# Kernel tuning notes

Hardware: AMD Instinct MI355X
Metric: run time of the kernel (lower is better)

Reference implementation:

```python
import jax, jax.numpy as jnp
import numpy as np

NUM_GROUPS = 32
EPS = 1e-6


def group_norm(x, gamma, beta):
    # x: [b, c, n]
    b, c, n = x.shape
    xg = x.reshape(b, NUM_GROUPS, (c // NUM_GROUPS) * n)
    mean = xg.mean(axis=-1, keepdims=True)
    var = xg.var(axis=-1, keepdims=True)
    xg = (xg - mean) * jax.lax.rsqrt(var + EPS)
    x = xg.reshape(b, c, n)
    return x * gamma[None, :, None] + beta[None, :, None]


def conv1x1(x, w, bias):
    # x: [b, c, n], w: [out, in], bias: [out]
    return jnp.einsum('oc,bcn->bon', w, x) + bias[None, :, None]


def setup_inputs() -> dict:
    key = jax.random.key(0)
    ks = jax.random.split(key, 12)
    b, c, n = 16, 512, 2048
    scale = 1.0 / np.sqrt(c)
    inp = {
        'x': jax.random.normal(ks[0], (b, c, n), dtype=jnp.float32),
        'gn_gamma': jnp.ones((c,), dtype=jnp.float32),
        'gn_beta': jnp.zeros((c,), dtype=jnp.float32),
        'wq': jax.random.normal(ks[1], (c, c), dtype=jnp.float32) * scale,
        'bq': jnp.zeros((c,), dtype=jnp.float32),
        'wk': jax.random.normal(ks[2], (c, c), dtype=jnp.float32) * scale,
        'bk': jnp.zeros((c,), dtype=jnp.float32),
        'wv': jax.random.normal(ks[3], (c, c), dtype=jnp.float32) * scale,
        'bv': jnp.zeros((c,), dtype=jnp.float32),
        'wo': jax.random.normal(ks[4], (c, c), dtype=jnp.float32) * scale,
        'bo': jnp.zeros((c,), dtype=jnp.float32),
    }
    return inp


def reference(x, gn_gamma, gn_beta, wq, bq, wk, bk, wv, bv, wo, bo):
    # x: [b, c, n]
    c = x.shape[1]
    h = group_norm(x, gn_gamma, gn_beta)
    q = conv1x1(h, wq, bq)  # [b, c, n]
    k = conv1x1(h, wk, bk)  # [b, c, n]
    v = conv1x1(h, wv, bv)  # [b, c, n]
    # scores: q^T k  -> [b, n_q, n_kv]
    scores = jnp.einsum('bcn,bcm->bnm', q, k) * (c ** -0.5)
    attn = jax.nn.softmax(scores, axis=-1)  # softmax over keys (dim=2)
    # h = v @ attn^T  -> [b, c, n_q]
    out = jnp.einsum('bcm,bnm->bcn', v, attn)
    out = conv1x1(out, wo, bo)
    return x + out
```

## Files before the change

### kernel.cpp

```cpp
#include <hip/hip_runtime.h>
#include <hip/hip_bf16.h>
#include <math.h>

#define Bb 16
#define Cc 512
#define Nn 2048

typedef unsigned short u16;
typedef __attribute__((ext_vector_type(8))) short bf16x8;
typedef __attribute__((ext_vector_type(4))) float f32x4;

typedef __attribute__((address_space(3))) unsigned as3_u32;
typedef __attribute__((address_space(1))) const unsigned as1_u32;

__device__ __forceinline__ float b2f(u16 u){ unsigned x = ((unsigned)u) << 16; return __builtin_bit_cast(float, x); }
__device__ __forceinline__ u16 f2b(float f){
  unsigned x = __builtin_bit_cast(unsigned, f);
  x += 0x7fffu + ((x >> 16) & 1u);
  return (u16)(x >> 16);
}

__device__ __forceinline__ void gload16(const u16* g, u16* l){
  __builtin_amdgcn_global_load_lds((as1_u32*)(uintptr_t)(const void*)g,
                                   (as3_u32*)(uintptr_t)(void*)l, 16, 0, 0);
}

#define BAR() do{ __builtin_amdgcn_s_barrier(); asm volatile("" ::: "memory"); }while(0)
#define WAITV4() asm volatile("s_waitcnt vmcnt(4)" ::: "memory")
#define WAITV0() asm volatile("s_waitcnt vmcnt(0)" ::: "memory")

__global__ __launch_bounds__(256) void k_cvt4(const float* __restrict__ s0, const float* __restrict__ s1,
                                              const float* __restrict__ s2, const float* __restrict__ s3,
                                              u16* __restrict__ d0, u16* __restrict__ d1,
                                              u16* __restrict__ d2, u16* __restrict__ d3){
  int z = blockIdx.z;
  const float* s = (z == 0) ? s0 : (z == 1) ? s1 : (z == 2) ? s2 : s3;
  u16* d = (z == 0) ? d0 : (z == 1) ? d1 : (z == 2) ? d2 : d3;
  int i = blockIdx.x * 256 + threadIdx.x;
  float4 v = ((const float4*)s)[i];
  ushort4 o; o.x = f2b(v.x); o.y = f2b(v.y); o.z = f2b(v.z); o.w = f2b(v.w);
  ((ushort4*)d)[i] = o;
}

__global__ __launch_bounds__(256) void k_gn(const float* __restrict__ x,
                                            const float* __restrict__ gamma,
                                            const float* __restrict__ beta,
                                            u16* __restrict__ h){
  int bid = blockIdx.x;
  int b = bid >> 5, g = bid & 31;
  const float4* xv = (const float4*)(x + ((size_t)b * Cc + g * 16) * Nn);
  u16* hp = h + ((size_t)b * Cc + g * 16) * Nn;
  int t = threadIdx.x;
  float s = 0.f, ss = 0.f;
#pragma unroll 4
  for (int it = 0; it < 32; ++it){
    float4 v = xv[it * 256 + t];
    s  += v.x + v.y + v.z + v.w;
    ss += v.x * v.x + v.y * v.y + v.z * v.z + v.w * v.w;
  }
#pragma unroll
  for (int o = 32; o >= 1; o >>= 1){ s += __shfl_xor(s, o); ss += __shfl_xor(ss, o); }
  __shared__ float rs[4], rss[4];
  int w = t >> 6;
  if ((t & 63) == 0){ rs[w] = s; rss[w] = ss; }
  __syncthreads();
  s  = rs[0] + rs[1] + rs[2] + rs[3];
  ss = rss[0] + rss[1] + rss[2] + rss[3];
  float mean = s * (1.f / 32768.f);
  float var  = ss * (1.f / 32768.f) - mean * mean;
  float inv  = rsqrtf(var + 1e-6f);
#pragma unroll 4
  for (int it = 0; it < 32; ++it){
    int idx = it * 256 + t;
    float4 u = xv[idx];
    int ch = g * 16 + (idx >> 9);
    float ga = gamma[ch] * inv, be = beta[ch];
    ushort4 o;
    o.x = f2b((u.x - mean) * ga + be);
    o.y = f2b((u.y - mean) * ga + be);
    o.z = f2b((u.z - mean) * ga + be);
    o.w = f2b((u.w - mean) * ga + be);
    ((ushort4*)hp)[idx] = o;
  }
}

__global__ __launch_bounds__(256) void k_tr(const u16* __restrict__ h, u16* __restrict__ ht){
  __shared__ u16 lds[64 * 65];
  int b = blockIdx.z;
  int n0 = blockIdx.x * 64, c0 = blockIdx.y * 64;
  const u16* src = h + (size_t)b * Cc * Nn;
  u16* dst = ht + (size_t)b * Nn * Cc;
  int t = threadIdx.x;
  int jc = (t & 7) << 3;
  int r  = t >> 3;
#pragma unroll
  for (int it = 0; it < 2; ++it){
    int rr = r + it * 32;
    uint4 vv = *(const uint4*)(src + (size_t)(c0 + rr) * Nn + n0 + jc);
    u16* pv = (u16*)&vv;
#pragma unroll
    for (int e = 0; e < 8; ++e) lds[(jc + e) * 65 + rr] = pv[e];
  }
  __syncthreads();
#pragma unroll
  for (int it = 0; it < 2; ++it){
    int rn = r + it * 32;
    u16 tmp[8];
#pragma unroll
    for (int e = 0; e < 8; ++e) tmp[e] = lds[rn * 65 + jc + e];
    *(uint4*)(dst + (size_t)(n0 + rn) * Cc + c0 + jc) = *(const uint4*)tmp;
  }
}

#define GSLOT 32768

__device__ __forceinline__ void gemm256(const u16* __restrict__ A, int lda,
                                        const u16* __restrict__ B, int ldb, int K,
                                        u16* __restrict__ lds, f32x4 (&acc)[8][4]){
  const int tid = threadIdx.x;
  const int w = tid >> 6, lane = tid & 63;
  const int lr = lane & 15, lk = lane >> 4;
  const int wr = w >> 2, wc = w & 3;

  const int sw0 = ((lk    ) ^ (lr & 7)) << 3;
  const int sw1 = ((lk + 4) ^ (lr & 7)) << 3;
  const int arow = (wr * 128 + lr) * 64;
  const int brow = 16384 + (wc * 64 + lr) * 64;

  const int r0 = tid >> 3, c0 = tid & 7;
  const size_t offA0 = (size_t)r0 * lda + (size_t)((c0 ^ (r0 & 7)) << 3);
  const size_t offA1 = offA0 + (size_t)64 * lda;
  const size_t offB0 = (size_t)r0 * ldb + (size_t)((c0 ^ (r0 & 7)) << 3);
  const size_t offB1 = offB0 + (size_t)64 * ldb;
  const int d0 = tid * 8, d1 = tid * 8 + 4096;

#define STGA(h, T, bu) do{ const u16* gp = A + (size_t)(T) * 64 + (size_t)(h) * 128 * lda; \
    u16* lp = lds + (bu) * GSLOT + (h) * 8192; \
    gload16(gp + offA0, lp + d0); gload16(gp + offA1, lp + d1); }while(0)
#define STGB(h, T, bu) do{ const u16* gp = B + (size_t)(T) * 64 + (size_t)(h) * 128 * ldb; \
    u16* lp = lds + (bu) * GSLOT + 16384 + (h) * 8192; \
    gload16(gp + offB0, lp + d0); gload16(gp + offB1, lp + d1); }while(0)

#pragma unroll
  for (int i = 0; i < 8; ++i)
#pragma unroll
    for (int j = 0; j < 4; ++j){ f32x4 z = {0.f,0.f,0.f,0.f}; acc[i][j] = z; }

  const int NT = K >> 6;

  STGA(0, 0, 0); STGA(1, 0, 0); STGB(0, 0, 0); STGB(1, 0, 0);
  if (NT > 1){ STGB(0, 1, 1); STGA(0, 1, 1); WAITV4(); }
  else { WAITV0(); }
  BAR();

  bf16x8 a[4][2], b[4][2];

#pragma unroll 1
  for (int T = 0; T < NT; ++T){
    const u16* cur = lds + (T & 1) * GSLOT;
    const int nb = (T + 1) & 1, cb = T & 1;
    const bool p1 = (T + 1) < NT, p2 = (T + 2) < NT;

#pragma unroll
    for (int i = 0; i < 4; ++i){
      a[i][0] = *(const bf16x8*)(cur + arow + i * 1024 + sw0);
      a[i][1] = *(const bf16x8*)(cur + arow + i * 1024 + sw1);
    }
#pragma unroll
    for (int j = 0; j < 2; ++j){
      b[j][0] = *(const bf16x8*)(cur + brow + j * 1024 + sw0);
      b[j][1] = *(const bf16x8*)(cur + brow + j * 1024 + sw1);
    }
    if (p1) STGB(1, T + 1, nb);
    BAR();
    __builtin_amdgcn_s_setprio(1);
#pragma unroll
    for (int i = 0; i < 4; ++i)
#pragma unroll
      for (int j = 0; j < 2; ++j)
#pragma unroll
        for (int ks = 0; ks < 2; ++ks)
          acc[i][j] = __builtin_amdgcn_mfma_f32_16x16x32_bf16(b[j][ks], a[i][ks], acc[i][j], 0, 0, 0);
    __builtin_amdgcn_s_setprio(0);
    BAR();

#pragma unroll
    for (int j = 2; j < 4; ++j){
      b[j][0] = *(const bf16x8*)(cur + brow + j * 1024 + sw0);
      b[j][1] = *(const bf16x8*)(cur + brow + j * 1024 + sw1);
    }
    if (p1) STGA(1, T + 1, nb);
    BAR();
    __builtin_amdgcn_s_setprio(1);
#pragma unroll
    for (int i = 0; i < 4; ++i)
#pragma unroll
      for (int j = 2; j < 4; ++j)
#pragma unroll
        for (int ks = 0; ks < 2; ++ks)
          acc[i][j] = __builtin_amdgcn_mfma_f32_16x16x32_bf16(b[j][ks], a[i][ks], acc[i][j], 0, 0, 0);
    __builtin_amdgcn_s_setprio(0);
    BAR();

#pragma unroll
    for (int i = 0; i < 4; ++i){
      a[i][0] = *(const bf16x8*)(cur + arow + 4096 + i * 1024 + sw0);
      a[i][1] = *(const bf16x8*)(cur + arow + 4096 + i * 1024 + sw1);
    }
    if (p2) STGB(0, T + 2, cb);
    BAR();
    __builtin_amdgcn_s_setprio(1);
#pragma unroll
    for (int i = 0; i < 4; ++i)
#pragma unroll
      for (int j = 0; j < 2; ++j)
#pragma unroll
        for (int ks = 0; ks < 2; ++ks)
          acc[4 + i][j] = __builtin_amdgcn_mfma_f32_16x16x32_bf16(b[j][ks], a[i][ks], acc[4 + i][j], 0, 0, 0);
    __builtin_amdgcn_s_setprio(0);
    BAR();

    if (p2) STGA(0, T + 2, cb);
    BAR();
    __builtin_amdgcn_s_setprio(1);
#pragma unroll
    for (int i = 0; i < 4; ++i)
#pragma unroll
      for (int j = 2; j < 4; ++j)
#pragma unroll
        for (int ks = 0; ks < 2; ++ks)
          acc[4 + i][j] = __builtin_amdgcn_mfma_f32_16x16x32_bf16(b[j][ks], a[i][ks], acc[4 + i][j], 0, 0, 0);
    __builtin_amdgcn_s_setprio(0);
    if (p2){ WAITV4(); } else if (p1){ WAITV0(); }
    BAR();
  }
#undef STGA
#undef STGB
}

#define EPI_COORDS \
  int lane = threadIdx.x & 63, w = threadIdx.x >> 6; \
  int wr = w >> 2, wc = w & 3; \
  int lr = lane & 15; \
  int lk = lane >> 4; \
  int g4 = lk << 2; \
  (void)lk;

__global__ __launch_bounds__(512, 2) void k_qkv(const u16* __restrict__ ht,
                                                const u16* __restrict__ wqb, const u16* __restrict__ wkb,
                                                const u16* __restrict__ wvb,
                                                const float* __restrict__ bq, const float* __restrict__ bk,
                                                const float* __restrict__ bv,
                                                u16* __restrict__ qt, u16* __restrict__ kt,
                                                u16* __restrict__ v){
  __shared__ u16 lds[2 * GSLOT];
  int bid = blockIdx.x;
  int id = (bid & 7) * 96 + (bid >> 3);
  f32x4 acc[8][4];
  if (id < 512){
    int b = id >> 5, r = id & 31;
    int p = r >> 4, t = r & 15;
    int m0 = (t & 7) * 256, n0 = (t >> 3) * 256;
    const u16* A = ht + (size_t)b * Nn * Cc + (size_t)m0 * Cc;
    const u16* B = (p ? wkb : wqb) + (size_t)n0 * Cc;
    const float* bias = p ? bk : bq;
    u16* out = (p ? kt : qt) + (size_t)b * Nn * Cc;
    gemm256(A, Cc, B, Cc, Cc, lds, acc);
    EPI_COORDS
#pragma unroll
    for (int i = 0; i < 8; ++i){
      int row = m0 + wr * 128 + i * 16 + lr;
#pragma unroll
      for (int j = 0; j < 4; ++j){
        int coln = n0 + wc * 64 + j * 16 + g4;
        float4 bi = *(const float4*)(bias + coln);
        ushort4 o;
        o.x = f2b(acc[i][j][0] + bi.x);
        o.y = f2b(acc[i][j][1] + bi.y);
        o.z = f2b(acc[i][j][2] + bi.z);
        o.w = f2b(acc[i][j][3] + bi.w);
        *(ushort4*)(out + (size_t)row * Cc + coln) = o;
      }
    }
  } else {
    int u = id - 512;
    int b = u >> 4, r = u & 15;
    int m0 = (r & 1) * 256, n0 = (r >> 1) * 256;
    const u16* A = wvb + (size_t)m0 * Cc;
    const u16* B = ht + (size_t)b * Nn * Cc + (size_t)n0 * Cc;
    u16* out = v + (size_t)b * Cc * Nn;
    gemm256(A, Cc, B, Cc, Cc, lds, acc);
    EPI_COORDS
#pragma unroll
    for (int i = 0; i < 8; ++i){
      int row = m0 + wr * 128 + i * 16 + lr;
      float bi = bv[row];
#pragma unroll
      for (int j = 0; j < 4; ++j){
        int coln = n0 + wc * 64 + j * 16 + g4;
        ushort4 o;
        o.x = f2b(acc[i][j][0] + bi);
        o.y = f2b(acc[i][j][1] + bi);
        o.z = f2b(acc[i][j][2] + bi);
        o.w = f2b(acc[i][j][3] + bi);
        *(ushort4*)(out + (size_t)row * Nn + coln) = o;
      }
    }
  }
}

__global__ __launch_bounds__(512, 2) void k_scores(const u16* __restrict__ qt, const u16* __restrict__ kt,
                                                   u16* __restrict__ p, float* __restrict__ lsum){
  __shared__ u16 lds[2 * GSLOT];
  __shared__ float sums[256][4];
  int bid = blockIdx.x;
  int swz = (bid & 7) * 128 + (bid >> 3);
  int b = swz >> 6, rem = swz & 63;
  int m0 = (rem & 7) * 256, n0 = (rem >> 3) * 256;
  const u16* A = qt + (size_t)b * Nn * Cc + (size_t)m0 * Cc;
  const u16* B = kt + (size_t)b * Nn * Cc + (size_t)n0 * Cc;
  u16* pb = p + (size_t)b * Nn * Nn;
  f32x4 acc[8][4];
  gemm256(A, Cc, B, Cc, Cc, lds, acc);
  const float scale = 0.044194173824159216f;
  EPI_COORDS
  float psum[8];
#pragma unroll
  for (int i = 0; i < 8; ++i) psum[i] = 0.f;
#pragma unroll
  for (int i = 0; i < 8; ++i){
    int row = m0 + wr * 128 + i * 16 + lr;
#pragma unroll
    for (int j = 0; j < 4; ++j){
      int coln = n0 + wc * 64 + j * 16 + g4;
      float e0 = __expf(acc[i][j][0] * scale);
      float e1 = __expf(acc[i][j][1] * scale);
      float e2 = __expf(acc[i][j][2] * scale);
      float e3 = __expf(acc[i][j][3] * scale);
      psum[i] += (e0 + e1) + (e2 + e3);
      ushort4 o; o.x = f2b(e0); o.y = f2b(e1); o.z = f2b(e2); o.w = f2b(e3);
      *(ushort4*)(pb + (size_t)row * Nn + coln) = o;
    }
  }
#pragma unroll
  for (int i = 0; i < 8; ++i){
    psum[i] += __shfl_xor(psum[i], 16);
    psum[i] += __shfl_xor(psum[i], 32);
  }
  if (lk == 0){
#pragma unroll
    for (int i = 0; i < 8; ++i) sums[wr * 128 + i * 16 + lr][wc] = psum[i];
  }
  __syncthreads();
  int tid = threadIdx.x;
  if (tid < 256){
    float sv = sums[tid][0] + sums[tid][1] + sums[tid][2] + sums[tid][3];
    atomicAdd(lsum + (size_t)b * Nn + m0 + tid, sv);
  }
}

__global__ __launch_bounds__(512, 2) void k_pv(const u16* __restrict__ p, const u16* __restrict__ v,
                                               const float* __restrict__ lsum, u16* __restrict__ aot){
  __shared__ u16 lds[2 * GSLOT];
  int bid = blockIdx.x;
  int swz = (bid & 7) * 32 + (bid >> 3);
  int b = swz >> 4, rem = swz & 15;
  int m0 = (rem & 7) * 256, n0 = (rem >> 3) * 256;
  const u16* A = p + (size_t)b * Nn * Nn + (size_t)m0 * Nn;
  const u16* B = v + (size_t)b * Cc * Nn + (size_t)n0 * Nn;
  u16* out = aot + (size_t)b * Nn * Cc;
  f32x4 acc[8][4];
  gemm256(A, Nn, B, Nn, Nn, lds, acc);
  EPI_COORDS
#pragma unroll
  for (int i = 0; i < 8; ++i){
    int row = m0 + wr * 128 + i * 16 + lr;
    float linv = 1.0f / lsum[(size_t)b * Nn + row];
#pragma unroll
    for (int j = 0; j < 4; ++j){
      int coln = n0 + wc * 64 + j * 16 + g4;
      ushort4 o;
      o.x = f2b(acc[i][j][0] * linv);
      o.y = f2b(acc[i][j][1] * linv);
      o.z = f2b(acc[i][j][2] * linv);
      o.w = f2b(acc[i][j][3] * linv);
      *(ushort4*)(out + (size_t)row * Cc + coln) = o;
    }
  }
}

__global__ __launch_bounds__(512, 2) void k_proj(const u16* __restrict__ wob, const u16* __restrict__ aot,
                                                 const float* __restrict__ bo, const float* __restrict__ x,
                                                 float* __restrict__ out){
  __shared__ u16 lds[2 * GSLOT];
  int b = blockIdx.z;
  int m0 = blockIdx.x * 256, n0 = blockIdx.y * 256;
  const u16* A = wob + (size_t)m0 * Cc;
  const u16* B = aot + (size_t)b * Nn * Cc + (size_t)n0 * Cc;
  f32x4 acc[8][4];
  gemm256(A, Cc, B, Cc, Cc, lds, acc);
  size_t base = (size_t)b * Cc * Nn;
  EPI_COORDS
#pragma unroll
  for (int i = 0; i < 8; ++i){
    int row = m0 + wr * 128 + i * 16 + lr;
    float bi = bo[row];
#pragma unroll
    for (int j = 0; j < 4; ++j){
      int coln = n0 + wc * 64 + j * 16 + g4;
      size_t idx = base + (size_t)row * Nn + coln;
      float4 xv = *(const float4*)(x + idx);
      float4 o;
      o.x = xv.x + bi + acc[i][j][0];
      o.y = xv.y + bi + acc[i][j][1];
      o.z = xv.z + bi + acc[i][j][2];
      o.w = xv.w + bi + acc[i][j][3];
      *(float4*)(out + idx) = o;
    }
  }
}

extern "C" void kernel_launch(void* const* d_in, const int* in_sizes, int n_in,
                              void* d_out, int out_size, void* d_ws, size_t ws_size,
                              hipStream_t stream){
  const float* x     = (const float*)d_in[0];
  const float* gamma = (const float*)d_in[1];
  const float* beta  = (const float*)d_in[2];
  const float* wq = (const float*)d_in[3];
  const float* bq = (const float*)d_in[4];
  const float* wk = (const float*)d_in[5];
  const float* bk = (const float*)d_in[6];
  const float* wv = (const float*)d_in[7];
  const float* bv = (const float*)d_in[8];
  const float* wo = (const float*)d_in[9];
  const float* bo = (const float*)d_in[10];
  float* out = (float*)d_out;

  char* ws = (char*)d_ws;
  const size_t MB = 1048576ull;
  u16* P   = (u16*)ws;
  u16* h   = (u16*)ws;
  u16* ht  = (u16*)(ws + 32 * MB);
  u16* wqb = (u16*)(ws + 64 * MB);
  u16* wkb = wqb + 262144;
  u16* wvb = wqb + 524288;
  u16* qt  = (u16*)(ws + 128 * MB);
  u16* kt  = (u16*)(ws + 160 * MB);
  u16* v   = (u16*)(ws + 192 * MB);
  u16* wob = (u16*)(ws + 224 * MB);
  float* lsum = (float*)(ws + 225 * MB);
  u16* aot = qt;

  k_cvt4<<<dim3(256, 1, 4), 256, 0, stream>>>(wq, wk, wv, wo, wqb, wkb, wvb, wob);
  k_gn<<<dim3(512), 256, 0, stream>>>(x, gamma, beta, h);
  k_tr<<<dim3(32, 8, 16), 256, 0, stream>>>(h, ht);
  k_qkv<<<dim3(768), 512, 0, stream>>>(ht, wqb, wkb, wvb, bq, bk, bv, qt, kt, v);
  hipMemsetAsync(lsum, 0, (size_t)Bb * Nn * sizeof(float), stream);
  k_scores<<<dim3(1024), 512, 0, stream>>>(qt, kt, P, lsum);
  k_pv<<<dim3(256), 512, 0, stream>>>(P, v, lsum, aot);
  k_proj<<<dim3(2, 8, 16), 512, 0, stream>>>(wob, aot, bo, x, out);
}
```

Before: 328.0 us.

## Store attention probabilities and V in FP8 and run PV GEMM on FP8 MFMA

The scores kernel now writes unnormalized exp probabilities as e4m3 bytes instead of bf16, and the V projection writes V as signed e4m3. The PV kernel gets its own FP8 GEMM mainloop with a swizzled LDS layout, a two-stage global-to-LDS prefetch and 16x16x32 fp8 MFMAs. This halves the bytes of the large P matrix written and read and doubles MFMA throughput for the PV product. In exchange, probabilities and V lose precision: exp values below 2^-6 flush to zero, since the conversion has no subnormal handling, and large values saturate, so accuracy against the reference may suffer.

```diff
diff --git a/kernel.cpp b/kernel.cpp
--- a/kernel.cpp
+++ b/kernel.cpp
@@ -7,6 +7,7 @@
 #define Nn 2048
 
 typedef unsigned short u16;
+typedef unsigned char u8;
 typedef __attribute__((ext_vector_type(8))) short bf16x8;
 typedef __attribute__((ext_vector_type(4))) float f32x4;
 
@@ -20,13 +21,35 @@
   return (u16)(x >> 16);
 }
 
+__device__ __forceinline__ unsigned f2e4m3(float f){
+  unsigned y = __builtin_bit_cast(unsigned, f);
+  if (y < 0x3C800000u) return 0u;
+  unsigned r = y - (120u << 23);
+  unsigned v = (r + 0x7FFFFu + ((r >> 20) & 1u)) >> 20;
+  return v > 0x7Eu ? 0x7Eu : v;
+}
+__device__ __forceinline__ unsigned f2e4m3s(float f){
+  unsigned y = __builtin_bit_cast(unsigned, f);
+  unsigned s = (y >> 24) & 0x80u;
+  y &= 0x7FFFFFFFu;
+  if (y < 0x3C800000u) return s;
+  unsigned r = y - (120u << 23);
+  unsigned v = (r + 0x7FFFFu + ((r >> 20) & 1u)) >> 20;
+  return s | (v > 0x7Eu ? 0x7Eu : v);
+}
+
 __device__ __forceinline__ void gload16(const u16* g, u16* l){
   __builtin_amdgcn_global_load_lds((as1_u32*)(uintptr_t)(const void*)g,
                                    (as3_u32*)(uintptr_t)(void*)l, 16, 0, 0);
 }
+__device__ __forceinline__ void gload16b(const u8* g, u8* l){
+  __builtin_amdgcn_global_load_lds((as1_u32*)(uintptr_t)(const void*)g,
+                                   (as3_u32*)(uintptr_t)(void*)l, 16, 0, 0);
+}
 
 #define BAR() do{ __builtin_amdgcn_s_barrier(); asm volatile("" ::: "memory"); }while(0)
 #define WAITV4() asm volatile("s_waitcnt vmcnt(4)" ::: "memory")
+#define WAITV2() asm volatile("s_waitcnt vmcnt(2)" ::: "memory")
 #define WAITV0() asm volatile("s_waitcnt vmcnt(0)" ::: "memory")
 
 __global__ __launch_bounds__(256) void k_cvt4(const float* __restrict__ s0, const float* __restrict__ s1,
@@ -252,7 +275,7 @@
                                                 const float* __restrict__ bq, const float* __restrict__ bk,
                                                 const float* __restrict__ bv,
                                                 u16* __restrict__ qt, u16* __restrict__ kt,
-                                                u16* __restrict__ v){
+                                                u8* __restrict__ v){
   __shared__ u16 lds[2 * GSLOT];
   int bid = blockIdx.x;
   int id = (bid & 7) * 96 + (bid >> 3);
@@ -288,7 +311,7 @@
     int m0 = (r & 1) * 256, n0 = (r >> 1) * 256;
     const u16* A = wvb + (size_t)m0 * Cc;
     const u16* B = ht + (size_t)b * Nn * Cc + (size_t)n0 * Cc;
-    u16* out = v + (size_t)b * Cc * Nn;
+    u8* out = v + (size_t)b * Cc * Nn;
     gemm256(A, Cc, B, Cc, Cc, lds, acc);
     EPI_COORDS
 #pragma unroll
@@ -298,19 +321,18 @@
 #pragma unroll
       for (int j = 0; j < 4; ++j){
         int coln = n0 + wc * 64 + j * 16 + g4;
-        ushort4 o;
-        o.x = f2b(acc[i][j][0] + bi);
-        o.y = f2b(acc[i][j][1] + bi);
-        o.z = f2b(acc[i][j][2] + bi);
-        o.w = f2b(acc[i][j][3] + bi);
-        *(ushort4*)(out + (size_t)row * Nn + coln) = o;
+        unsigned o = f2e4m3s(acc[i][j][0] + bi)
+                   | (f2e4m3s(acc[i][j][1] + bi) << 8)
+                   | (f2e4m3s(acc[i][j][2] + bi) << 16)
+                   | (f2e4m3s(acc[i][j][3] + bi) << 24);
+        *(unsigned*)(out + (size_t)row * Nn + coln) = o;
       }
     }
   }
 }
 
 __global__ __launch_bounds__(512, 2) void k_scores(const u16* __restrict__ qt, const u16* __restrict__ kt,
-                                                   u16* __restrict__ p, float* __restrict__ lsum){
+                                                   u8* __restrict__ p, float* __restrict__ lsum){
   __shared__ u16 lds[2 * GSLOT];
   __shared__ float sums[256][4];
   int bid = blockIdx.x;
@@ -319,7 +341,7 @@
   int m0 = (rem & 7) * 256, n0 = (rem >> 3) * 256;
   const u16* A = qt + (size_t)b * Nn * Cc + (size_t)m0 * Cc;
   const u16* B = kt + (size_t)b * Nn * Cc + (size_t)n0 * Cc;
-  u16* pb = p + (size_t)b * Nn * Nn;
+  u8* pb = p + (size_t)b * Nn * Nn;
   f32x4 acc[8][4];
   gemm256(A, Cc, B, Cc, Cc, lds, acc);
   const float scale = 0.044194173824159216f;
@@ -338,8 +360,8 @@
       float e2 = __expf(acc[i][j][2] * scale);
       float e3 = __expf(acc[i][j][3] * scale);
       psum[i] += (e0 + e1) + (e2 + e3);
-      ushort4 o; o.x = f2b(e0); o.y = f2b(e1); o.z = f2b(e2); o.w = f2b(e3);
-      *(ushort4*)(pb + (size_t)row * Nn + coln) = o;
+      unsigned o = f2e4m3(e0) | (f2e4m3(e1) << 8) | (f2e4m3(e2) << 16) | (f2e4m3(e3) << 24);
+      *(unsigned*)(pb + (size_t)row * Nn + coln) = o;
     }
   }
 #pragma unroll
@@ -359,19 +381,148 @@
   }
 }
 
-__global__ __launch_bounds__(512, 2) void k_pv(const u16* __restrict__ p, const u16* __restrict__ v,
+__global__ __launch_bounds__(512, 2) void k_pv(const u8* __restrict__ p, const u8* __restrict__ v,
                                                const float* __restrict__ lsum, u16* __restrict__ aot){
-  __shared__ u16 lds[2 * GSLOT];
+  __shared__ u8 lds[2 * 32768];
   int bid = blockIdx.x;
   int swz = (bid & 7) * 32 + (bid >> 3);
   int b = swz >> 4, rem = swz & 15;
   int m0 = (rem & 7) * 256, n0 = (rem >> 3) * 256;
-  const u16* A = p + (size_t)b * Nn * Nn + (size_t)m0 * Nn;
-  const u16* B = v + (size_t)b * Cc * Nn + (size_t)n0 * Nn;
+  const u8* A = p + (size_t)b * Nn * Nn + (size_t)m0 * Nn;
+  const u8* B = v + (size_t)b * Cc * Nn + (size_t)n0 * Nn;
   u16* out = aot + (size_t)b * Nn * Cc;
+
+  const int tid = threadIdx.x;
+  const int w = tid >> 6, lane = tid & 63;
+  const int lr = lane & 15, lk = lane >> 4;
+  const int wr = w >> 2, wc = w & 3;
+
+  int aofs[8][2], bofs[4][2];
+#pragma unroll
+  for (int i = 0; i < 8; ++i){
+    int row = wr * 128 + i * 16 + lr;
+    int sz = (row & 3) ^ ((row >> 2) & 3);
+#pragma unroll
+    for (int ks = 0; ks < 2; ++ks)
+      aofs[i][ks] = row * 64 + ((((ks << 1) | (lk >> 1)) ^ sz) << 4) + ((lk & 1) << 3);
+  }
+#pragma unroll
+  for (int j = 0; j < 4; ++j){
+    int row = wc * 64 + j * 16 + lr;
+    int sz = (row & 3) ^ ((row >> 2) & 3);
+#pragma unroll
+    for (int ks = 0; ks < 2; ++ks)
+      bofs[j][ks] = 16384 + row * 64 + ((((ks << 1) | (lk >> 1)) ^ sz) << 4) + ((lk & 1) << 3);
+  }
+
+  const int srow = tid >> 2, sc = tid & 3;
+  const int ssz = (srow & 3) ^ ((srow >> 2) & 3);
+  const size_t offS = (size_t)srow * Nn + (size_t)((sc ^ ssz) << 4);
+  const int sdst = tid * 16;
+
+#define PSTGA(h, T, bu) gload16b(A + (size_t)(T) * 64 + (size_t)(h) * 128 * Nn + offS, \
+                                 lds + (bu) * 32768 + (h) * 8192 + sdst)
+#define PSTGB(h, T, bu) gload16b(B + (size_t)(T) * 64 + (size_t)(h) * 128 * Nn + offS, \
+                                 lds + (bu) * 32768 + 16384 + (h) * 8192 + sdst)
+
   f32x4 acc[8][4];
-  gemm256(A, Nn, B, Nn, Nn, lds, acc);
-  EPI_COORDS
+#pragma unroll
+  for (int i = 0; i < 8; ++i)
+#pragma unroll
+    for (int j = 0; j < 4; ++j){ f32x4 z = {0.f,0.f,0.f,0.f}; acc[i][j] = z; }
+
+  const int NT = Nn >> 6;
+
+  PSTGA(0, 0, 0); PSTGA(1, 0, 0); PSTGB(0, 0, 0); PSTGB(1, 0, 0);
+  PSTGB(0, 1, 1); PSTGA(0, 1, 1);
+  WAITV2();
+  BAR();
+
+  long a[4][2], bf[4][2];
+
+#pragma unroll 1
+  for (int T = 0; T < NT; ++T){
+    const u8* cur = lds + (T & 1) * 32768;
+    const int nb = (T + 1) & 1, cb = T & 1;
+    const bool p1 = (T + 1) < NT, p2 = (T + 2) < NT;
+
+#pragma unroll
+    for (int i = 0; i < 4; ++i){
+      a[i][0] = *(const long*)(cur + aofs[i][0]);
+      a[i][1] = *(const long*)(cur + aofs[i][1]);
+    }
+#pragma unroll
+    for (int j = 0; j < 2; ++j){
+      bf[j][0] = *(const long*)(cur + bofs[j][0]);
+      bf[j][1] = *(const long*)(cur + bofs[j][1]);
+    }
+    if (p1) PSTGB(1, T + 1, nb);
+    BAR();
+    __builtin_amdgcn_s_setprio(1);
+#pragma unroll
+    for (int i = 0; i < 4; ++i)
+#pragma unroll
+      for (int j = 0; j < 2; ++j)
+#pragma unroll
+        for (int ks = 0; ks < 2; ++ks)
+          acc[i][j] = __builtin_amdgcn_mfma_f32_16x16x32_fp8_fp8(bf[j][ks], a[i][ks], acc[i][j], 0, 0, 0);
+    __builtin_amdgcn_s_setprio(0);
+    BAR();
+
+#pragma unroll
+    for (int j = 2; j < 4; ++j){
+      bf[j][0] = *(const long*)(cur + bofs[j][0]);
+      bf[j][1] = *(const long*)(cur + bofs[j][1]);
+    }
+    if (p1) PSTGA(1, T + 1, nb);
+    BAR();
+    __builtin_amdgcn_s_setprio(1);
+#pragma unroll
+    for (int i = 0; i < 4; ++i)
+#pragma unroll
+      for (int j = 2; j < 4; ++j)
+#pragma unroll
+        for (int ks = 0; ks < 2; ++ks)
+          acc[i][j] = __builtin_amdgcn_mfma_f32_16x16x32_fp8_fp8(bf[j][ks], a[i][ks], acc[i][j], 0, 0, 0);
+    __builtin_amdgcn_s_setprio(0);
+    BAR();
+
+#pragma unroll
+    for (int i = 0; i < 4; ++i){
+      a[i][0] = *(const long*)(cur + aofs[4 + i][0]);
+      a[i][1] = *(const long*)(cur + aofs[4 + i][1]);
+    }
+    if (p2) PSTGB(0, T + 2, cb);
+    BAR();
+    __builtin_amdgcn_s_setprio(1);
+#pragma unroll
+    for (int i = 0; i < 4; ++i)
+#pragma unroll
+      for (int j = 0; j < 2; ++j)
+#pragma unroll
+        for (int ks = 0; ks < 2; ++ks)
+          acc[4 + i][j] = __builtin_amdgcn_mfma_f32_16x16x32_fp8_fp8(bf[j][ks], a[i][ks], acc[4 + i][j], 0, 0, 0);
+    __builtin_amdgcn_s_setprio(0);
+    BAR();
+
+    if (p2) PSTGA(0, T + 2, cb);
+    BAR();
+    __builtin_amdgcn_s_setprio(1);
+#pragma unroll
+    for (int i = 0; i < 4; ++i)
+#pragma unroll
+      for (int j = 2; j < 4; ++j)
+#pragma unroll
+        for (int ks = 0; ks < 2; ++ks)
+          acc[4 + i][j] = __builtin_amdgcn_mfma_f32_16x16x32_fp8_fp8(bf[j][ks], a[i][ks], acc[4 + i][j], 0, 0, 0);
+    __builtin_amdgcn_s_setprio(0);
+    if (p2){ WAITV2(); } else if (p1){ WAITV0(); }
+    BAR();
+  }
+#undef PSTGA
+#undef PSTGB
+
+  int g4 = lk << 2;
 #pragma unroll
   for (int i = 0; i < 8; ++i){
     int row = m0 + wr * 128 + i * 16 + lr;
@@ -438,7 +589,7 @@
 
   char* ws = (char*)d_ws;
   const size_t MB = 1048576ull;
-  u16* P   = (u16*)ws;
+  u8*  P   = (u8*)ws;
   u16* h   = (u16*)ws;
   u16* ht  = (u16*)(ws + 32 * MB);
   u16* wqb = (u16*)(ws + 64 * MB);
@@ -446,7 +597,7 @@
   u16* wvb = wqb + 524288;
   u16* qt  = (u16*)(ws + 128 * MB);
   u16* kt  = (u16*)(ws + 160 * MB);
-  u16* v   = (u16*)(ws + 192 * MB);
+  u8*  v   = (u8*)(ws + 192 * MB);
   u16* wob = (u16*)(ws + 224 * MB);
   float* lsum = (float*)(ws + 225 * MB);
   u16* aot = qt;
```

Measured after the change: 307.8 us (median of 2 runs). 6.2% less time.
